# Optimization experiments

Hardware: AMD Instinct MI355X
Metric: run time of the kernel (lower is better)

## Reference

```python
import jax, jax.numpy as jnp
import numpy as np

B, T, D, H, C = 256, 512, 128, 512, 10

def setup_inputs() -> dict:
    key = jax.random.key(0)
    ks = jax.random.split(key, 12)
    s_x = 1.0 / np.sqrt(D)
    s_h = 1.0 / np.sqrt(H)
    inp = {
        'x':   jax.random.normal(ks[0], (B, T, D), dtype=jnp.float32),
        'wgx': jax.random.normal(ks[1], (D, H), dtype=jnp.float32) * s_x,
        'wgh': jax.random.normal(ks[2], (H, H), dtype=jnp.float32) * s_h,
        'bg':  jnp.zeros((H,), dtype=jnp.float32),
        'wix': jax.random.normal(ks[3], (D, H), dtype=jnp.float32) * s_x,
        'wih': jax.random.normal(ks[4], (H, H), dtype=jnp.float32) * s_h,
        'bi':  jnp.zeros((H,), dtype=jnp.float32),
        'wfx': jax.random.normal(ks[5], (D, H), dtype=jnp.float32) * s_x,
        'wfh': jax.random.normal(ks[6], (H, H), dtype=jnp.float32) * s_h,
        'bf':  jnp.ones((H,), dtype=jnp.float32),  # forget bias = 1 as in source
        'wox': jax.random.normal(ks[7], (D, H), dtype=jnp.float32) * s_x,
        'woh': jax.random.normal(ks[8], (H, H), dtype=jnp.float32) * s_h,
        'bo':  jnp.zeros((H,), dtype=jnp.float32),
        'wph': jax.random.normal(ks[9], (H, C), dtype=jnp.float32) * s_h,
        'bp':  jnp.zeros((C,), dtype=jnp.float32),
    }
    return inp

def reference(x, wgx, wgh, bg, wix, wih, bi, wfx, wfh, bf, wox, woh, bo, wph, bp):
    # Precompute all input projections as one big batched GEMM per gate: [B,T,H]
    xg = jnp.einsum('btd,dh->bth', x, wgx) + bg
    xi = jnp.einsum('btd,dh->bth', x, wix) + bi
    xf = jnp.einsum('btd,dh->bth', x, wfx) + bf
    xo = jnp.einsum('btd,dh->bth', x, wox) + bo

    def step(carry, xt):
        h_prev, c_prev = carry
        xg_t, xi_t, xf_t, xo_t = xt
        gt = jnp.tanh(xg_t + h_prev @ wgh)
        it = jax.nn.sigmoid(xi_t + h_prev @ wih)
        ft = jax.nn.sigmoid(xf_t + h_prev @ wfh)
        ot = jax.nn.sigmoid(xo_t + h_prev @ woh)
        ct = gt * it + c_prev * ft
        ht = jnp.tanh(ct) * ot
        return (ht, ct), None

    h0 = jnp.zeros((x.shape[0], wgh.shape[0]), dtype=x.dtype)
    c0 = jnp.zeros_like(h0)
    # scan over time: move T to leading axis
    xs = (xg.swapaxes(0, 1), xi.swapaxes(0, 1), xf.swapaxes(0, 1), xo.swapaxes(0, 1))
    (hT, _), _ = jax.lax.scan(step, (h0, c0), xs)
    return hT @ wph + bp
```

## Files before the change

### kernel.cpp

```cpp
#include <hip/hip_runtime.h>
#include <hip/hip_bf16.h>
#include <stdint.h>

typedef __attribute__((ext_vector_type(8))) short short8;
typedef __attribute__((ext_vector_type(4))) float floatx4;
typedef __attribute__((ext_vector_type(4))) int intx4;
typedef __attribute__((ext_vector_type(4))) unsigned int uintx4;
typedef __attribute__((ext_vector_type(4))) unsigned short ushort4v;

#define DEVI __device__ __forceinline__

constexpr int B_ = 256, T_ = 512, D_ = 128, H_ = 512, C_ = 10;
constexpr int KTOT = H_ + D_;
constexpr int RG = 16;
constexpr int NBG = 16;
constexpr int NCG = 16;
constexpr int HCW = 32;

constexpr size_t OFF_XB = 0;
constexpr size_t SZ_XB  = (size_t)B_ * T_ * D_ * 2;
constexpr size_t OFF_WC = OFF_XB + SZ_XB;
constexpr size_t SZ_WC  = (size_t)4 * H_ * KTOT * 2;
constexpr size_t OFF_HB = OFF_WC + SZ_WC;
constexpr size_t SZ_HB  = (size_t)2 * B_ * H_ * 2;
constexpr size_t OFF_FL = OFF_HB + SZ_HB;
constexpr size_t SZ_FL  = (size_t)NBG * NCG * 64;
constexpr size_t WS_NEED = OFF_FL + SZ_FL;

DEVI uint16_t f2bf(float f) {
    uint32_t u = __builtin_bit_cast(uint32_t, f);
    u += 0x7FFFu + ((u >> 16) & 1u);
    return (uint16_t)(u >> 16);
}
DEVI float bf2f(uint16_t u) {
    return __builtin_bit_cast(float, (uint32_t)u << 16);
}
DEVI float sigf(float x)  { return 1.0f / (1.0f + __expf(-x)); }
DEVI float tanhf_(float x){ return 1.0f - 2.0f / (1.0f + __expf(2.0f * x)); }

__global__ void k_cvt_x(const float* __restrict__ x, uint16_t* __restrict__ xb) {
    int i = (blockIdx.x * 256 + threadIdx.x) * 4;
    float4 v = *reinterpret_cast<const float4*>(x + i);
    ushort4v o;
    o.x = f2bf(v.x); o.y = f2bf(v.y); o.z = f2bf(v.z); o.w = f2bf(v.w);
    *reinterpret_cast<ushort4v*>(xb + i) = o;
}

__global__ void k_build_w(const float* __restrict__ wgh, const float* __restrict__ wih,
                          const float* __restrict__ wfh, const float* __restrict__ woh,
                          const float* __restrict__ wgx, const float* __restrict__ wix,
                          const float* __restrict__ wfx, const float* __restrict__ wox,
                          uint16_t* __restrict__ wc) {
    int np = blockIdx.x;
    int g = np >> 9, n = np & 511;
    const float* wh = (g == 0) ? wgh : (g == 1) ? wih : (g == 2) ? wfh : woh;
    const float* wx = (g == 0) ? wgx : (g == 1) ? wix : (g == 2) ? wfx : wox;
    for (int k = threadIdx.x; k < KTOT; k += 256) {
        float v = (k < H_) ? wh[(size_t)k * H_ + n] : wx[(size_t)(k - H_) * H_ + n];
        wc[(size_t)np * KTOT + k] = f2bf(v);
    }
}

#define WLOAD(dst, base, IMM) \
    asm volatile("global_load_dwordx4 %0, %1, off offset:" #IMM \
                 : "=v"(dst) : "v"(base))
#define WLOAD20(arr, base) \
    WLOAD(arr[0],  base, 0);    WLOAD(arr[1],  base, 64);   \
    WLOAD(arr[2],  base, 128);  WLOAD(arr[3],  base, 192);  \
    WLOAD(arr[4],  base, 256);  WLOAD(arr[5],  base, 320);  \
    WLOAD(arr[6],  base, 384);  WLOAD(arr[7],  base, 448);  \
    WLOAD(arr[8],  base, 512);  WLOAD(arr[9],  base, 576);  \
    WLOAD(arr[10], base, 640);  WLOAD(arr[11], base, 704);  \
    WLOAD(arr[12], base, 768);  WLOAD(arr[13], base, 832);  \
    WLOAD(arr[14], base, 896);  WLOAD(arr[15], base, 960);  \
    WLOAD(arr[16], base, 1024); WLOAD(arr[17], base, 1088); \
    WLOAD(arr[18], base, 1152); WLOAD(arr[19], base, 1216)

#define HLOAD(dst, base, IMM) \
    asm volatile("global_load_dwordx4 %0, %1, off offset:" #IMM " sc0 sc1" \
                 : "=v"(dst) : "v"(base) : "memory")

__global__ __launch_bounds__(256, 1) void k_lstm(
    const uint16_t* __restrict__ xb,
    const uint16_t* __restrict__ wc,
    const float* __restrict__ bgp, const float* __restrict__ bip,
    const float* __restrict__ bfp, const float* __restrict__ bop,
    uint16_t* hbuf,
    int* flags)
{
    __shared__ __align__(16) short hx[RG * KTOT];
    __shared__ float pre[4][RG][HCW + 2];

    const int tid  = threadIdx.x;
    const int lane = tid & 63;
    const int w    = tid >> 6;
    const int bid  = blockIdx.x;
    const int xcd = bid & 7, j = bid >> 3;
    const int bg = xcd * 2 + (j >> 4);
    const int cg = j & 15;
    const int b0  = bg * RG;
    const int hc0 = cg * HCW;

    short8 bfr0[20], bfr1[20];
    {
        const int lcol = lane & 15, kgrp = lane >> 4;
        const uint16_t* src0 = wc + (size_t)(w * H_ + hc0 + 0  + lcol) * KTOT + kgrp * 8;
        const uint16_t* src1 = wc + (size_t)(w * H_ + hc0 + 16 + lcol) * KTOT + kgrp * 8;
        WLOAD20(bfr0, src0);
        WLOAD20(bfr1, src1);
        asm volatile("s_waitcnt vmcnt(0)" ::: "memory");
    }

    const int erow = tid >> 4;
    const int epr  = tid & 15;
    const int hcg0 = hc0 + epr * 2;
    float bge[2], bie[2], bfe[2], boe[2], cst[2] = {0.f, 0.f};
    #pragma unroll
    for (int e = 0; e < 2; ++e) {
        bge[e] = bgp[hcg0 + e]; bie[e] = bip[hcg0 + e];
        bfe[e] = bfp[hcg0 + e]; boe[e] = bop[hcg0 + e];
    }

    const int srow = tid >> 4, sseg = tid & 15;
    const int sswz = (srow & 7) << 4;
    const int arow = lane & 15, akg = lane >> 4;
    const int abase = arow * (KTOT * 2) + akg * 16;
    const int aswz  = (arow & 7) << 4;

    int* fbase = flags + bg * NCG * 16;
    char* lds = (char*)hx;

    for (int t = 0; t < T_; ++t) {
        {
            const short8 xv = *reinterpret_cast<const short8*>(
                xb + ((size_t)(b0 + srow) * T_ + t) * D_ + sseg * 8);
            int byte = srow * (KTOT * 2) + H_ * 2 + sseg * 16;
            *reinterpret_cast<short8*>(lds + (byte ^ sswz)) = xv;
        }

        if (t > 0) {
            if (w == 0) {
                int it = 0;
                for (;;) {
                    int f = t;
                    if (lane < NCG)
                        f = __hip_atomic_load(fbase + lane * 16, __ATOMIC_RELAXED,
                                              __HIP_MEMORY_SCOPE_AGENT);
                    if (__ballot(f == t) == ~0ull) break;
                    if (++it > (1 << 22)) break;
                    __builtin_amdgcn_s_sleep(1);
                }
                asm volatile("" ::: "memory");
            }
            __syncthreads();
        }

        if (t == 0) {
            intx4 z = {0, 0, 0, 0};
            #pragma unroll
            for (int c4 = 0; c4 < 4; ++c4) {
                int byte = srow * (KTOT * 2) + sseg * 64 + c4 * 16;
                *reinterpret_cast<intx4*>(lds + (byte ^ sswz)) = z;
            }
        } else {
            const uint32_t* src = reinterpret_cast<const uint32_t*>(
                hbuf + (size_t)(t & 1) * B_ * H_ + (size_t)(b0 + srow) * H_ + sseg * 32);
            uintx4 v0, v1, v2, v3;
            HLOAD(v0, src, 0);  HLOAD(v1, src, 16);
            HLOAD(v2, src, 32); HLOAD(v3, src, 48);
            asm volatile("s_waitcnt vmcnt(0)" ::: "memory");
            #pragma unroll
            for (int c4 = 0; c4 < 4; ++c4) {
                uintx4 v = (c4 == 0) ? v0 : (c4 == 1) ? v1 : (c4 == 2) ? v2 : v3;
                int byte = srow * (KTOT * 2) + sseg * 64 + c4 * 16;
                *reinterpret_cast<uintx4*>(lds + (byte ^ sswz)) = v;
            }
        }
        __syncthreads();

        floatx4 acc0 = {0.f, 0.f, 0.f, 0.f}, acc1 = {0.f, 0.f, 0.f, 0.f};
        #pragma unroll
        for (int ks = 0; ks < 20; ++ks) {
            int byte = (abase + ks * 64) ^ aswz;
            short8 a = *reinterpret_cast<const short8*>(lds + byte);
            acc0 = __builtin_amdgcn_mfma_f32_16x16x32_bf16(a, bfr0[ks], acc0, 0, 0, 0);
            acc1 = __builtin_amdgcn_mfma_f32_16x16x32_bf16(a, bfr1[ks], acc1, 0, 0, 0);
        }
        #pragma unroll
        for (int r = 0; r < 4; ++r) {
            pre[w][(lane >> 4) * 4 + r][(lane & 15)]      = acc0[r];
            pre[w][(lane >> 4) * 4 + r][16 + (lane & 15)] = acc1[r];
        }
        __syncthreads();

        float hp[2];
        #pragma unroll
        for (int e = 0; e < 2; ++e) {
            int col = epr * 2 + e;
            float ag = pre[0][erow][col] + bge[e];
            float ai = pre[1][erow][col] + bie[e];
            float af = pre[2][erow][col] + bfe[e];
            float ao = pre[3][erow][col] + boe[e];
            float g = tanhf_(ag), ii = sigf(ai), f = sigf(af), o = sigf(ao);
            float c = g * ii + cst[e] * f;
            cst[e] = c;
            hp[e] = tanhf_(c) * o;
        }
        uint32_t packed = (uint32_t)f2bf(hp[0]) | ((uint32_t)f2bf(hp[1]) << 16);
        uint32_t* hdst = reinterpret_cast<uint32_t*>(
            hbuf + (size_t)((t + 1) & 1) * B_ * H_ + (size_t)(b0 + erow) * H_ + hcg0);
        __hip_atomic_store(hdst, packed, __ATOMIC_RELAXED, __HIP_MEMORY_SCOPE_AGENT);
        asm volatile("s_waitcnt vmcnt(0)" ::: "memory");
        __syncthreads();
        if (tid == 0)
            __hip_atomic_store(fbase + cg * 16, t + 1, __ATOMIC_RELAXED,
                               __HIP_MEMORY_SCOPE_AGENT);
    }
}

__global__ void k_proj(const uint16_t* __restrict__ hb0, const float* __restrict__ wph,
                       const float* __restrict__ bp, float* __restrict__ out) {
    int b = blockIdx.x, lane = threadIdx.x;
    const uint32_t* hrow = reinterpret_cast<const uint32_t*>(hb0 + (size_t)b * H_);
    float p[C_];
    #pragma unroll
    for (int c = 0; c < C_; ++c) p[c] = 0.f;
    #pragma unroll
    for (int q = 0; q < 4; ++q) {
        int k2 = lane + q * 64;
        uint32_t u = __hip_atomic_load(hrow + k2, __ATOMIC_RELAXED, __HIP_MEMORY_SCOPE_AGENT);
        float h0 = bf2f((uint16_t)(u & 0xFFFFu));
        float h1 = bf2f((uint16_t)(u >> 16));
        #pragma unroll
        for (int c = 0; c < C_; ++c)
            p[c] += h0 * wph[(size_t)(2 * k2) * C_ + c] + h1 * wph[(size_t)(2 * k2 + 1) * C_ + c];
    }
    #pragma unroll
    for (int c = 0; c < C_; ++c) {
        float v = p[c];
        #pragma unroll
        for (int off = 32; off; off >>= 1) v += __shfl_down(v, off, 64);
        if (lane == 0) out[(size_t)b * C_ + c] = v + bp[c];
    }
}

extern "C" void kernel_launch(void* const* d_in, const int* in_sizes, int n_in,
                              void* d_out, int out_size, void* d_ws, size_t ws_size,
                              hipStream_t stream) {
    const float* x   = (const float*)d_in[0];
    const float* wgx = (const float*)d_in[1];
    const float* wgh = (const float*)d_in[2];
    const float* bg  = (const float*)d_in[3];
    const float* wix = (const float*)d_in[4];
    const float* wih = (const float*)d_in[5];
    const float* bi  = (const float*)d_in[6];
    const float* wfx = (const float*)d_in[7];
    const float* wfh = (const float*)d_in[8];
    const float* bf  = (const float*)d_in[9];
    const float* wox = (const float*)d_in[10];
    const float* woh = (const float*)d_in[11];
    const float* bo  = (const float*)d_in[12];
    const float* wph = (const float*)d_in[13];
    const float* bp  = (const float*)d_in[14];

    if (ws_size < WS_NEED) return;

    char* ws = (char*)d_ws;
    uint16_t* xbp = (uint16_t*)(ws + OFF_XB);
    uint16_t* wcp = (uint16_t*)(ws + OFF_WC);
    uint16_t* hbp = (uint16_t*)(ws + OFF_HB);
    int*      flp = (int*)(ws + OFF_FL);

    hipMemsetAsync(flp, 0, SZ_FL, stream);
    k_cvt_x<<<(B_ * T_ * D_) / (256 * 4), 256, 0, stream>>>(x, xbp);
    k_build_w<<<4 * H_, 256, 0, stream>>>(wgh, wih, wfh, woh, wgx, wix, wfx, wox, wcp);
    k_lstm<<<256, 256, 0, stream>>>(xbp, wcp, bg, bi, bf, bo, hbp, flp);
    k_proj<<<B_, 64, 0, stream>>>(hbp , wph, bp, (float*)d_out);
}
```

Baseline: 1.345 ms.

## Replace per-step block barriers with per-wave polling and double-buffered LDS

Each wave now polls the cross-block step flags itself, instead of wave 0 polling and then a block barrier. The hidden-state and x tile is double-buffered in LDS so the next step's staging cannot clobber the tile still being read. An LDS wave-flag spin replaces the __syncthreads before the MFMA loop, and the x-part k-slices are issued first so they can start before h arrives. This is meant to cut barrier and serialization latency on the per-timestep critical path, at the cost of more spinning traffic and a more fragile hand-rolled intra-block sync.

Measured after the change: 1.594 ms. +18.5%, slower.

```diff
diff --git a/kernel.cpp b/kernel.cpp
--- a/kernel.cpp
+++ b/kernel.cpp
@@ -4,7 +4,6 @@
 
 typedef __attribute__((ext_vector_type(8))) short short8;
 typedef __attribute__((ext_vector_type(4))) float floatx4;
-typedef __attribute__((ext_vector_type(4))) int intx4;
 typedef __attribute__((ext_vector_type(4))) unsigned int uintx4;
 typedef __attribute__((ext_vector_type(4))) unsigned short ushort4v;
 
@@ -16,6 +15,7 @@
 constexpr int NBG = 16;
 constexpr int NCG = 16;
 constexpr int HCW = 32;
+constexpr int ROWB = RG * KTOT * 2;
 
 constexpr size_t OFF_XB = 0;
 constexpr size_t SZ_XB  = (size_t)B_ * T_ * D_ * 2;
@@ -88,8 +88,9 @@
     uint16_t* hbuf,
     int* flags)
 {
-    __shared__ __align__(16) short hx[RG * KTOT];
-    __shared__ float pre[4][RG][HCW + 2];
+    __shared__ __align__(16) char hx[2][ROWB];
+    __shared__ float pre[4][RG][HCW + 1];
+    __shared__ int waveflag[4];
 
     const int tid  = threadIdx.x;
     const int lane = tid & 63;
@@ -121,68 +122,80 @@
         bfe[e] = bfp[hcg0 + e]; boe[e] = bop[hcg0 + e];
     }
 
-    const int srow = tid >> 4, sseg = tid & 15;
-    const int sswz = (srow & 7) << 4;
-    const int arow = lane & 15, akg = lane >> 4;
-    const int abase = arow * (KTOT * 2) + akg * 16;
-    const int aswz  = (arow & 7) << 4;
+    const int row = lane & 15;
+    const int cb  = lane >> 4;
+    const int swz = (row & 7) << 4;
 
     int* fbase = flags + bg * NCG * 16;
-    char* lds = (char*)hx;
+    int* myflag = fbase + cg * 16;
+    const int* pollp = fbase + (w * 4 + (lane & 3)) * 16;
+
+    if (tid < 4) waveflag[tid] = -1;
+    __syncthreads();
 
     for (int t = 0; t < T_; ++t) {
+        char* buf = hx[t & 1];
+
+        const short8 xv = *reinterpret_cast<const short8*>(
+            xb + ((size_t)(b0 + row) * T_ + t) * D_ + w * 32 + cb * 8);
+
+        uintx4 v0, v1, v2, v3;
+        if (t > 0) {
+            int it = 0;
+            for (;;) {
+                int f = __hip_atomic_load(pollp, __ATOMIC_RELAXED, __HIP_MEMORY_SCOPE_AGENT);
+                if (__all(f >= t)) break;
+                if (++it > (1 << 22)) break;
+            }
+            asm volatile("" ::: "memory");
+            const uint16_t* hbase = hbuf + (size_t)(t & 1) * B_ * H_
+                                         + (size_t)(b0 + row) * H_ + w * 128 + cb * 8;
+            HLOAD(v0, hbase, 0);
+            HLOAD(v1, hbase, 64);
+            HLOAD(v2, hbase, 128);
+            HLOAD(v3, hbase, 192);
+        }
+        asm volatile("s_waitcnt vmcnt(0)" ::: "memory");
+
         {
-            const short8 xv = *reinterpret_cast<const short8*>(
-                xb + ((size_t)(b0 + srow) * T_ + t) * D_ + sseg * 8);
-            int byte = srow * (KTOT * 2) + H_ * 2 + sseg * 16;
-            *reinterpret_cast<short8*>(lds + (byte ^ sswz)) = xv;
-        }
-
+            int byte = row * (KTOT * 2) + 1024 + w * 64 + cb * 16;
+            *reinterpret_cast<short8*>(buf + (byte ^ swz)) = xv;
+        }
         if (t > 0) {
-            if (w == 0) {
-                int it = 0;
-                for (;;) {
-                    int f = t;
-                    if (lane < NCG)
-                        f = __hip_atomic_load(fbase + lane * 16, __ATOMIC_RELAXED,
-                                              __HIP_MEMORY_SCOPE_AGENT);
-                    if (__ballot(f == t) == ~0ull) break;
-                    if (++it > (1 << 22)) break;
-                    __builtin_amdgcn_s_sleep(1);
-                }
-                asm volatile("" ::: "memory");
-            }
-            __syncthreads();
-        }
-
-        if (t == 0) {
-            intx4 z = {0, 0, 0, 0};
             #pragma unroll
-            for (int c4 = 0; c4 < 4; ++c4) {
-                int byte = srow * (KTOT * 2) + sseg * 64 + c4 * 16;
-                *reinterpret_cast<intx4*>(lds + (byte ^ sswz)) = z;
+            for (int i = 0; i < 4; ++i) {
+                uintx4 v = (i == 0) ? v0 : (i == 1) ? v1 : (i == 2) ? v2 : v3;
+                int byte = row * (KTOT * 2) + (w * 4 + i) * 64 + cb * 16;
+                *reinterpret_cast<uintx4*>(buf + (byte ^ swz)) = v;
             }
         } else {
-            const uint32_t* src = reinterpret_cast<const uint32_t*>(
-                hbuf + (size_t)(t & 1) * B_ * H_ + (size_t)(b0 + srow) * H_ + sseg * 32);
-            uintx4 v0, v1, v2, v3;
-            HLOAD(v0, src, 0);  HLOAD(v1, src, 16);
-            HLOAD(v2, src, 32); HLOAD(v3, src, 48);
-            asm volatile("s_waitcnt vmcnt(0)" ::: "memory");
+            uintx4 z = {0u, 0u, 0u, 0u};
             #pragma unroll
-            for (int c4 = 0; c4 < 4; ++c4) {
-                uintx4 v = (c4 == 0) ? v0 : (c4 == 1) ? v1 : (c4 == 2) ? v2 : v3;
-                int byte = srow * (KTOT * 2) + sseg * 64 + c4 * 16;
-                *reinterpret_cast<uintx4*>(lds + (byte ^ sswz)) = v;
-            }
-        }
-        __syncthreads();
+            for (int i = 0; i < 4; ++i) {
+                int byte = row * (KTOT * 2) + (w * 4 + i) * 64 + cb * 16;
+                *reinterpret_cast<uintx4*>(buf + (byte ^ swz)) = z;
+            }
+        }
+        __hip_atomic_store(&waveflag[w], t, __ATOMIC_RELEASE, __HIP_MEMORY_SCOPE_WORKGROUP);
+
+        {
+            volatile int* wf = (volatile int*)waveflag;
+            int it = 0;
+            for (;;) {
+                int f0 = wf[0], f1 = wf[1], f2 = wf[2], f3 = wf[3];
+                if (f0 >= t && f1 >= t && f2 >= t && f3 >= t) break;
+                if (++it > (1 << 25)) break;
+            }
+            asm volatile("" ::: "memory");
+            __builtin_amdgcn_sched_barrier(0);
+        }
 
         floatx4 acc0 = {0.f, 0.f, 0.f, 0.f}, acc1 = {0.f, 0.f, 0.f, 0.f};
         #pragma unroll
-        for (int ks = 0; ks < 20; ++ks) {
-            int byte = (abase + ks * 64) ^ aswz;
-            short8 a = *reinterpret_cast<const short8*>(lds + byte);
+        for (int i = 0; i < 20; ++i) {
+            const int ks = (i < 4) ? (16 + i) : (i - 4);
+            int byte = (row * (KTOT * 2) + ks * 64 + cb * 16) ^ swz;
+            short8 a = *reinterpret_cast<const short8*>(buf + byte);
             acc0 = __builtin_amdgcn_mfma_f32_16x16x32_bf16(a, bfr0[ks], acc0, 0, 0, 0);
             acc1 = __builtin_amdgcn_mfma_f32_16x16x32_bf16(a, bfr1[ks], acc1, 0, 0, 0);
         }
@@ -213,8 +226,7 @@
         asm volatile("s_waitcnt vmcnt(0)" ::: "memory");
         __syncthreads();
         if (tid == 0)
-            __hip_atomic_store(fbase + cg * 16, t + 1, __ATOMIC_RELAXED,
-                               __HIP_MEMORY_SCOPE_AGENT);
+            __hip_atomic_store(myflag, t + 1, __ATOMIC_RELAXED, __HIP_MEMORY_SCOPE_AGENT);
     }
 }
 
```

## Remap gate columns per wave to drop LDS gate exchange and extra barriers

Applied to the files above, without the earlier changes.

Weight rows are remapped so each wave computes all four gates for its own 8 hidden columns, letting the LSTM cell update use lane shuffles instead of a shared-memory pre-activation buffer and its __syncthreads. Every wave now polls the cross-block flags itself, using >= with no sleep, which removes the barrier after the wait. This shortens the serial per-timestep critical path of the persistent recurrent kernel. In exchange, all four waves spin on global atomics, which adds memory traffic, and the output store pattern changes to rows paired via shuffles.

After: 1.445 ms. +7.4%, slower.

```diff
diff --git a/kernel.cpp b/kernel.cpp
--- a/kernel.cpp
+++ b/kernel.cpp
@@ -4,7 +4,6 @@
 
 typedef __attribute__((ext_vector_type(8))) short short8;
 typedef __attribute__((ext_vector_type(4))) float floatx4;
-typedef __attribute__((ext_vector_type(4))) int intx4;
 typedef __attribute__((ext_vector_type(4))) unsigned int uintx4;
 typedef __attribute__((ext_vector_type(4))) unsigned short ushort4v;
 
@@ -88,8 +87,7 @@
     uint16_t* hbuf,
     int* flags)
 {
-    __shared__ __align__(16) short hx[RG * KTOT];
-    __shared__ float pre[4][RG][HCW + 2];
+    __shared__ __align__(16) char hx[RG * KTOT * 2];
 
     const int tid  = threadIdx.x;
     const int lane = tid & 63;
@@ -104,22 +102,21 @@
     short8 bfr0[20], bfr1[20];
     {
         const int lcol = lane & 15, kgrp = lane >> 4;
-        const uint16_t* src0 = wc + (size_t)(w * H_ + hc0 + 0  + lcol) * KTOT + kgrp * 8;
-        const uint16_t* src1 = wc + (size_t)(w * H_ + hc0 + 16 + lcol) * KTOT + kgrp * 8;
+        const int cw = lcol & 7, hi2 = lcol >> 3;
+        const int colg = hc0 + w * 8 + cw;
+        const uint16_t* src0 = wc + (size_t)((0 + hi2) * H_ + colg) * KTOT + kgrp * 8;
+        const uint16_t* src1 = wc + (size_t)((2 + hi2) * H_ + colg) * KTOT + kgrp * 8;
         WLOAD20(bfr0, src0);
         WLOAD20(bfr1, src1);
         asm volatile("s_waitcnt vmcnt(0)" ::: "memory");
     }
 
-    const int erow = tid >> 4;
-    const int epr  = tid & 15;
-    const int hcg0 = hc0 + epr * 2;
-    float bge[2], bie[2], bfe[2], boe[2], cst[2] = {0.f, 0.f};
-    #pragma unroll
-    for (int e = 0; e < 2; ++e) {
-        bge[e] = bgp[hcg0 + e]; bie[e] = bip[hcg0 + e];
-        bfe[e] = bfp[hcg0 + e]; boe[e] = bop[hcg0 + e];
-    }
+    const int cl   = lane & 7;
+    const bool lo  = (lane & 8) == 0;
+    const int rb   = (lane >> 4) * 4 + (lo ? 0 : 2);
+    const int mycol = hc0 + w * 8 + cl;
+    const float bgv = bgp[mycol], biv = bip[mycol], bfv = bfp[mycol], bov = bop[mycol];
+    float cst[2] = {0.f, 0.f};
 
     const int srow = tid >> 4, sseg = tid & 15;
     const int sswz = (srow & 7) << 4;
@@ -128,7 +125,8 @@
     const int aswz  = (arow & 7) << 4;
 
     int* fbase = flags + bg * NCG * 16;
-    char* lds = (char*)hx;
+    int* myflag = fbase + cg * 16;
+    char* lds = hx;
 
     for (int t = 0; t < T_; ++t) {
         {
@@ -138,31 +136,26 @@
             *reinterpret_cast<short8*>(lds + (byte ^ sswz)) = xv;
         }
 
-        if (t > 0) {
-            if (w == 0) {
+        if (t == 0) {
+            uintx4 z = {0u, 0u, 0u, 0u};
+            #pragma unroll
+            for (int c4 = 0; c4 < 4; ++c4) {
+                int byte = srow * (KTOT * 2) + sseg * 64 + c4 * 16;
+                *reinterpret_cast<uintx4*>(lds + (byte ^ sswz)) = z;
+            }
+        } else {
+            {
                 int it = 0;
                 for (;;) {
                     int f = t;
                     if (lane < NCG)
                         f = __hip_atomic_load(fbase + lane * 16, __ATOMIC_RELAXED,
                                               __HIP_MEMORY_SCOPE_AGENT);
-                    if (__ballot(f == t) == ~0ull) break;
+                    if (__ballot(f >= t) == ~0ull) break;
                     if (++it > (1 << 22)) break;
-                    __builtin_amdgcn_s_sleep(1);
                 }
                 asm volatile("" ::: "memory");
             }
-            __syncthreads();
-        }
-
-        if (t == 0) {
-            intx4 z = {0, 0, 0, 0};
-            #pragma unroll
-            for (int c4 = 0; c4 < 4; ++c4) {
-                int byte = srow * (KTOT * 2) + sseg * 64 + c4 * 16;
-                *reinterpret_cast<intx4*>(lds + (byte ^ sswz)) = z;
-            }
-        } else {
             const uint32_t* src = reinterpret_cast<const uint32_t*>(
                 hbuf + (size_t)(t & 1) * B_ * H_ + (size_t)(b0 + srow) * H_ + sseg * 32);
             uintx4 v0, v1, v2, v3;
@@ -186,35 +179,44 @@
             acc0 = __builtin_amdgcn_mfma_f32_16x16x32_bf16(a, bfr0[ks], acc0, 0, 0, 0);
             acc1 = __builtin_amdgcn_mfma_f32_16x16x32_bf16(a, bfr1[ks], acc1, 0, 0, 0);
         }
+
+        float q0[4], q1[4];
         #pragma unroll
         for (int r = 0; r < 4; ++r) {
-            pre[w][(lane >> 4) * 4 + r][(lane & 15)]      = acc0[r];
-            pre[w][(lane >> 4) * 4 + r][16 + (lane & 15)] = acc1[r];
-        }
-        __syncthreads();
-
-        float hp[2];
+            q0[r] = __shfl_xor(acc0[r], 8, 64);
+            q1[r] = __shfl_xor(acc1[r], 8, 64);
+        }
+        float hpair[2];
         #pragma unroll
         for (int e = 0; e < 2; ++e) {
-            int col = epr * 2 + e;
-            float ag = pre[0][erow][col] + bge[e];
-            float ai = pre[1][erow][col] + bie[e];
-            float af = pre[2][erow][col] + bfe[e];
-            float ao = pre[3][erow][col] + boe[e];
-            float g = tanhf_(ag), ii = sigf(ai), f = sigf(af), o = sigf(ao);
+            float pg = lo ? acc0[e] : q0[2 + e];
+            float pi = lo ? q0[e]   : acc0[2 + e];
+            float pf = lo ? acc1[e] : q1[2 + e];
+            float po = lo ? q1[e]   : acc1[2 + e];
+            float g = tanhf_(pg + bgv), ii = sigf(pi + biv);
+            float f = sigf(pf + bfv),   o  = sigf(po + bov);
             float c = g * ii + cst[e] * f;
             cst[e] = c;
-            hp[e] = tanhf_(c) * o;
-        }
-        uint32_t packed = (uint32_t)f2bf(hp[0]) | ((uint32_t)f2bf(hp[1]) << 16);
+            hpair[e] = tanhf_(c) * o;
+        }
+        float p0 = __shfl_xor(hpair[0], 1, 64);
+        float p1 = __shfl_xor(hpair[1], 1, 64);
+        uint32_t word; int strow;
+        if ((cl & 1) == 0) {
+            word = (uint32_t)f2bf(hpair[0]) | ((uint32_t)f2bf(p0) << 16);
+            strow = rb;
+        } else {
+            word = (uint32_t)f2bf(p1) | ((uint32_t)f2bf(hpair[1]) << 16);
+            strow = rb + 1;
+        }
         uint32_t* hdst = reinterpret_cast<uint32_t*>(
-            hbuf + (size_t)((t + 1) & 1) * B_ * H_ + (size_t)(b0 + erow) * H_ + hcg0);
-        __hip_atomic_store(hdst, packed, __ATOMIC_RELAXED, __HIP_MEMORY_SCOPE_AGENT);
+            hbuf + (size_t)((t + 1) & 1) * B_ * H_
+                 + (size_t)(b0 + strow) * H_ + hc0 + w * 8 + (cl & ~1));
+        __hip_atomic_store(hdst, word, __ATOMIC_RELAXED, __HIP_MEMORY_SCOPE_AGENT);
         asm volatile("s_waitcnt vmcnt(0)" ::: "memory");
         __syncthreads();
         if (tid == 0)
-            __hip_atomic_store(fbase + cg * 16, t + 1, __ATOMIC_RELAXED,
-                               __HIP_MEMORY_SCOPE_AGENT);
+            __hip_atomic_store(myflag, t + 1, __ATOMIC_RELAXED, __HIP_MEMORY_SCOPE_AGENT);
     }
 }
 
```
